# Performance work log

Measured on AMD Instinct MI355X. Metric: run time of the kernel, lower is better.

Reference implementation:

```python
import jax, jax.numpy as jnp
import numpy as np

N_USERS, N_ITEMS, DIM = 50000, 25000, 128
E_H, E_R = 600000, 1000000
N_LAYERS = 2


def setup_inputs() -> dict:
    key = jax.random.key(0)
    ks = jax.random.split(key, 20)
    nrm = lambda k, s: jax.random.normal(k, s, jnp.float32) * 0.05
    inp = {
        "u_emb": nrm(ks[0], (N_USERS, DIM)),
        "i_emb": nrm(ks[1], (N_ITEMS, DIM)),
        "gating_W": nrm(ks[2], (4, DIM, DIM)),
        "gating_b": jnp.zeros((4, DIM), jnp.float32),
        "attention": nrm(ks[3], (DIM,)),
        "attention_mat": nrm(ks[4], (DIM, DIM)),
    }
    for i, name in enumerate(["Hs", "Hj", "Hp"]):
        inp[name + "_row"] = jax.random.randint(ks[5 + 2 * i], (E_H,), 0, N_USERS, jnp.int32)
        inp[name + "_col"] = jax.random.randint(ks[6 + 2 * i], (E_H,), 0, N_USERS, jnp.int32)
        inp[name + "_val"] = jax.random.uniform(ks[11 + i], (E_H,), jnp.float32)
    inp["R_row"] = jax.random.randint(ks[14], (E_R,), 0, N_USERS, jnp.int32)
    inp["R_col"] = jax.random.randint(ks[15], (E_R,), 0, N_ITEMS, jnp.int32)
    inp["R_val"] = jnp.ones((E_R,), jnp.float32)
    return inp


def spmm(row, col, val, X, n_out):
    # sparse (n_out x n_in) @ dense (n_in x d), COO edge list form
    return jax.ops.segment_sum(val[:, None] * X[col], row, num_segments=n_out)


def l2norm(x):
    return x * jax.lax.rsqrt(jnp.maximum(jnp.sum(x * x, axis=1, keepdims=True), 1e-12))


def reference(u_emb, i_emb, gating_W, gating_b, attention, attention_mat,
              Hs_row, Hs_col, Hs_val, Hj_row, Hj_col, Hj_val,
              Hp_row, Hp_col, Hp_val, R_row, R_col, R_val):
    gate = lambda e, c: e * jax.nn.sigmoid(e @ gating_W[c] + gating_b[c])

    def chan_att(cs):
        # per-channel attention score: sum_d a_d * (E_c @ W_att)_d  -> [N, C]
        w = jnp.stack([jnp.sum(attention * (c @ attention_mat), axis=1) for c in cs], axis=1)
        s = jax.nn.softmax(w, axis=1)
        mixed = sum(s[:, k:k + 1] * cs[k] for k in range(len(cs)))
        return mixed, s

    H = [(Hs_row, Hs_col, Hs_val), (Hj_row, Hj_col, Hj_val), (Hp_row, Hp_col, Hp_val)]
    cur = [gate(u_emb, c) for c in range(3)]        # channel user embeddings
    cur_s = gate(u_emb, 3)                          # simple-gated user embeddings
    cur_i = i_emb
    all_c = [[cur[k]] for k in range(3)]
    all_i = [cur_i]
    all_s = [cur_s]
    for _ in range(N_LAYERS):
        mixed = chan_att(cur)[0] + cur_s / 2
        for k in range(3):
            r, c, v = H[k]
            cur[k] = spmm(r, c, v, cur[k], N_USERS)
            all_c[k].append(l2norm(cur[k]))
        new_item = spmm(R_col, R_row, R_val, mixed, N_ITEMS)   # R^T @ mixed
        all_i.append(l2norm(new_item))
        cur_s = spmm(R_row, R_col, R_val, cur_i, N_USERS)      # R @ item
        all_s.append(l2norm(cur_s))
        cur_i = new_item
    fc = [sum(all_c[k]) for k in range(3)]
    final_user = chan_att(fc)[0] + sum(all_s) / 2
    final_item = sum(all_i)
    return jnp.concatenate([final_user, final_item], axis=0)  # [N_USERS+N_ITEMS, DIM]
```

## Files before the change

kernel.cpp:

```cpp
#include <hip/hip_runtime.h>
#include <cstddef>
#include <cstdint>

#define NU 50000
#define NI 25000
#define DIMN 128
#define EH 600000
#define ER 1000000

typedef unsigned int u32;
typedef unsigned long long u64;
typedef unsigned char u8;
typedef __attribute__((ext_vector_type(8))) short short8;
typedef __attribute__((ext_vector_type(16))) float float16;

__device__ __forceinline__ float wave_sum64(float v) {
#pragma unroll
  for (int m = 32; m >= 1; m >>= 1) v += __shfl_xor(v, m, 64);
  return v;
}

__device__ __forceinline__ u32 pack_bf16x2(float a, float b) {
  u32 ua = __float_as_uint(a), ub = __float_as_uint(b);
  ua = (ua + 0x7fffu + ((ua >> 16) & 1u)) >> 16;
  ub = (ub + 0x7fffu + ((ub >> 16) & 1u)) >> 16;
  return ua | (ub << 16);
}
__device__ __forceinline__ u32 bf16_hi(float v) {
  u32 u = __float_as_uint(v);
  u = (u + 0x7fffu + ((u >> 16) & 1u)) & 0xffff0000u;
  return u;
}
__device__ __forceinline__ float blo(u32 p) { return __uint_as_float(p << 16); }
__device__ __forceinline__ float bhi(u32 p) { return __uint_as_float(p & 0xffff0000u); }

struct Graphs {
  const int* row[5];
  const int* col[5];
  const float* val[5];
};

__device__ __forceinline__ int g_E(int z) {
  const int E[5] = {EH, EH, EH, ER, ER};
  return E[z];
}

#define NBKU 196
#define TOTB (5 * NBKU)
#define CAPH 3584
#define CAPR 5632
#define CAPT 5632
#define ECAP 4315136
#define FCAP 5760
#define CHUNK 2048

__device__ __forceinline__ int capstart(int z, int b) {
  const int base[5] = {0, 702464, 1404928, 2107392, 3211264};
  const int cap[5] = {CAPH, CAPH, CAPH, CAPR, CAPT};
  return base[z] + b * cap[z];
}

__global__ __launch_bounds__(256) void k_prep(const float* __restrict__ U, u32* __restrict__ UP16,
                                              const float* __restrict__ IE,
                                              float* __restrict__ out_i, u32* __restrict__ IE16,
                                              const float* __restrict__ W, u32* __restrict__ W16,
                                              const float* __restrict__ attm,
                                              const float* __restrict__ att,
                                              float* __restrict__ attv) {
  int b = blockIdx.x;
  if (b < 12500) {
    int i = b * 256 + threadIdx.x;
    float2 v = ((const float2*)U)[i];
    UP16[i] = pack_bf16x2(v.x, v.y);
  } else if (b < 18750) {
    int i = (b - 12500) * 256 + threadIdx.x;
    float2 v = ((const float2*)IE)[i];
    ((float2*)out_i)[i] = v;
    IE16[i] = pack_bf16x2(v.x, v.y);
  } else if (b < 18878) {
    int i = (b - 18750) * 256 + threadIdx.x;
    int col = i & 127, k2 = (i >> 7) & 63, c = i >> 13;
    const float* Wc = W + (size_t)c * DIMN * DIMN;
    W16[i] = pack_bf16x2(Wc[(size_t)(2 * k2) * DIMN + col], Wc[(size_t)(2 * k2 + 1) * DIMN + col]);
  } else {
    int e = threadIdx.x;
    if (e < 128) {
      float s = 0.f;
      for (int d = 0; d < DIMN; ++d) s += attm[e * DIMN + d] * att[d];
      attv[e] = s;
    }
  }
}

__global__ __launch_bounds__(256) void k_gate(const u32* __restrict__ UP16,
                                              const u32* __restrict__ W16,
                                              const float* __restrict__ B, u32* S16, u32* G016,
                                              u32* G116, u32* G216) {
  int c = blockIdx.y;
  const u32* __restrict__ Wc = W16 + (size_t)c * (64 * 128);
  int r0 = blockIdx.x * 64;
  int t = threadIdx.x;
  int w = t >> 6, lane = t & 63;
  int ln = lane & 31, h = lane >> 5;
  int rh = w & 1, mh = w >> 1;

  __shared__ u32 ldsP[64 * 65];

  int rowl = rh * 32 + ln;
  int rg = r0 + rowl;
  int rc = (rg < NU) ? rg : (NU - 1);

  float16 acc[2];
#pragma unroll
  for (int m = 0; m < 2; ++m)
#pragma unroll
    for (int q = 0; q < 16; ++q) acc[m][q] = 0.f;

  const u32* __restrict__ urow = UP16 + (size_t)rc * 64;
#pragma unroll
  for (int kk = 0; kk < 8; ++kk) {
    int kw = kk * 8 + 4 * h;
    union {
      u32 u[4];
      short8 s;
    } bf;
#pragma unroll
    for (int j = 0; j < 4; ++j) bf.u[j] = urow[kw + j];
#pragma unroll
    for (int m = 0; m < 2; ++m) {
      union {
        u32 u[4];
        short8 s;
      } af;
      int col = 64 * mh + 32 * m + ln;
#pragma unroll
      for (int j = 0; j < 4; ++j) af.u[j] = Wc[(size_t)(kw + j) * DIMN + col];
      acc[m] = __builtin_amdgcn_mfma_f32_32x32x16_bf16(af.s, bf.s, acc[m], 0, 0, 0);
    }
  }
#pragma unroll
  for (int m = 0; m < 2; ++m)
#pragma unroll
    for (int q = 0; q < 16; q += 2) {
      int cw = 32 * mh + 16 * m + ((q & 3) >> 1) + 4 * (q >> 2) + 2 * h;
      ldsP[rowl * 65 + cw] = pack_bf16x2(acc[m][q], acc[m][q + 1]);
    }
  __syncthreads();

  int colw = t & 63, rloc = t >> 6;
  float bx = B[c * DIMN + 2 * colw], by = B[c * DIMN + 2 * colw + 1];
  u32* dst = (c == 0) ? G016 : (c == 1) ? G116 : (c == 2) ? G216 : S16;
#pragma unroll
  for (int i = 0; i < 16; ++i) {
    int row = i * 4 + rloc;
    int rg2 = r0 + row;
    if (rg2 >= NU) continue;
    u32 p = ldsP[row * 65 + colw];
    u32 uu = UP16[(size_t)rg2 * 64 + colw];
    float sx = 1.f / (1.f + __expf(-(blo(p) + bx)));
    float sy = 1.f / (1.f + __expf(-(bhi(p) + by)));
    dst[(size_t)rg2 * 64 + colw] = pack_bf16x2(blo(uu) * sx, bhi(uu) * sy);
  }
}

__global__ __launch_bounds__(256) void k_bscat(Graphs g, int* __restrict__ bcnt,
                                               u32* __restrict__ epb, u8* __restrict__ erb) {
  int z = blockIdx.y;
  int E = g_E(z);
  if ((int)(blockIdx.x * CHUNK) >= E) return;
  int sh = (z == 4) ? 7 : 8;
  int mask = (1 << sh) - 1;
  __shared__ int hist[2][NBKU], basel[NBKU], curl[2][NBKU], h0s[NBKU];
  for (int i = threadIdx.x; i < NBKU; i += 256) {
    hist[0][i] = 0;
    hist[1][i] = 0;
    curl[0][i] = 0;
    curl[1][i] = 0;
  }
  __syncthreads();
  const int* __restrict__ row = g.row[z];
  const int* __restrict__ col = g.col[z];
  const float* __restrict__ val = g.val[z];
  int e0 = blockIdx.x * CHUNK + threadIdx.x;
  int half = threadIdx.x >> 7;
  int r[8];
  u32 pay[8];
  bool ok[8];
#pragma unroll
  for (int k = 0; k < 8; ++k) {
    int e = e0 + k * 256;
    ok[k] = e < E;
    r[k] = ok[k] ? row[e] : 0;
    pay[k] = ok[k] ? (u32)col[e] : 0u;
  }
  if (z < 3) {
#pragma unroll
    for (int k = 0; k < 8; ++k) {
      int e = e0 + k * 256;
      if (ok[k]) pay[k] |= bf16_hi(val[e]);
    }
  }
#pragma unroll
  for (int k = 0; k < 8; ++k)
    if (ok[k]) atomicAdd(&hist[half][r[k] >> sh], 1);
  __syncthreads();
  for (int i = threadIdx.x; i < NBKU; i += 256) {
    int h0 = hist[0][i];
    int tot = h0 + hist[1][i];
    h0s[i] = h0;
    if (tot) basel[i] = capstart(z, i) + atomicAdd(&bcnt[z * NBKU + i], tot);
  }
  __syncthreads();
#pragma unroll
  for (int k = 0; k < 8; ++k)
    if (ok[k]) {
      int b = r[k] >> sh;
      int rank = atomicAdd(&curl[half][b], 1);
      int pos = basel[b] + (half ? h0s[b] : 0) + rank;
      epb[pos] = pay[k];
      erb[pos] = (u8)(r[k] & mask);
    }
}

__global__ __launch_bounds__(256) void k_fine(u32* __restrict__ epb, const u8* __restrict__ erb,
                                              const int* __restrict__ bcnt,
                                              int* __restrict__ ptr2) {
  int z = blockIdx.y, b = blockIdx.x, t = threadIdx.x;
  int sh = (z == 4) ? 7 : 8;
  int mask = (1 << sh) - 1;
  const int poffs2[5] = {0, 100000, 200000, 300000, 400000};
  const int nz[5] = {NU, NU, NU, NU, NI};
  int s = capstart(z, b);
  int n = bcnt[z * NBKU + b];
  __shared__ int cnt[256], scn[256], curl[256];
  __shared__ u32 buf[FCAP];
  cnt[t] = 0;
  curl[t] = 0;
  __syncthreads();
  for (int i = t; i < n; i += 256) atomicAdd(&cnt[erb[s + i]], 1);
  __syncthreads();
  int v = cnt[t];
  scn[t] = v;
  __syncthreads();
  for (int o = 1; o < 256; o <<= 1) {
    int x = (t >= o) ? scn[t - o] : 0;
    __syncthreads();
    scn[t] += x;
    __syncthreads();
  }
  int excl = scn[t] - v;
  __syncthreads();
  scn[t] = excl;
  int rg = (b << sh) + t;
  if (t <= mask && rg < nz[z]) {
    ptr2[poffs2[z] + 2 * rg] = s + excl;
    ptr2[poffs2[z] + 2 * rg + 1] = s + excl + v;
  }
  __syncthreads();
  for (int i = t; i < n; i += 256) {
    int r = erb[s + i];
    int rank = atomicAdd(&curl[r], 1);
    buf[scn[r] + rank] = epb[s + i];
  }
  __syncthreads();
  for (int i = t; i < n; i += 256) epb[s + i] = buf[i];
}

struct Job {
  const int* ptr2;
  const u32* X16;
  u32* Y16;
  float* ACCF;
  u32* ACC16;
  const u32* AINIT16;
  int nrows;
};

template <bool UNIT>
__device__ __forceinline__ void spmm_run(const u32* __restrict__ ep, const Job& jb) {
  int w = blockIdx.x * 4 + __builtin_amdgcn_readfirstlane(threadIdx.x >> 6);
  int lane = threadIdx.x & 63;
  if (w >= jb.nrows) return;
  const int2 pp = ((const int2*)jb.ptr2)[w];
  int s = __builtin_amdgcn_readfirstlane(pp.x);
  int t = __builtin_amdgcn_readfirstlane(pp.y);
  const char* __restrict__ Xb = (const char*)jb.X16;
  u32 lo4 = (u32)(lane << 2);
  float ax = 0.f, ay = 0.f;
  int e = s;
  for (; e + 8 <= t; e += 8) {
    u32 off[8];
    float vv[8];
#pragma unroll
    for (int k = 0; k < 8; ++k) {
      u32 q = ep[e + k];
      if (UNIT) {
        off[k] = (q << 8) | lo4;
      } else {
        off[k] = ((q & 0xffffu) << 8) | lo4;
        vv[k] = bhi(q);
      }
    }
    u32 p[8];
#pragma unroll
    for (int k = 0; k < 8; ++k) p[k] = *(const u32*)(Xb + off[k]);
#pragma unroll
    for (int k = 0; k < 8; ++k) {
      if (UNIT) {
        ax += blo(p[k]);
        ay += bhi(p[k]);
      } else {
        ax += vv[k] * blo(p[k]);
        ay += vv[k] * bhi(p[k]);
      }
    }
  }
  for (; e + 4 <= t; e += 4) {
    u32 off[4];
    float vv[4];
#pragma unroll
    for (int k = 0; k < 4; ++k) {
      u32 q = ep[e + k];
      if (UNIT) {
        off[k] = (q << 8) | lo4;
      } else {
        off[k] = ((q & 0xffffu) << 8) | lo4;
        vv[k] = bhi(q);
      }
    }
    u32 p[4];
#pragma unroll
    for (int k = 0; k < 4; ++k) p[k] = *(const u32*)(Xb + off[k]);
#pragma unroll
    for (int k = 0; k < 4; ++k) {
      if (UNIT) {
        ax += blo(p[k]);
        ay += bhi(p[k]);
      } else {
        ax += vv[k] * blo(p[k]);
        ay += vv[k] * bhi(p[k]);
      }
    }
  }
  for (; e < t; ++e) {
    u32 q = ep[e];
    u32 off;
    float v = 1.f;
    if (UNIT) {
      off = (q << 8) | lo4;
    } else {
      off = ((q & 0xffffu) << 8) | lo4;
      v = bhi(q);
    }
    u32 p = *(const u32*)(Xb + off);
    ax += v * blo(p);
    ay += v * bhi(p);
  }
  size_t b64 = (size_t)w * 64 + lane;
  if (jb.ACCF) {
    float ss = wave_sum64(ax * ax + ay * ay);
    float rs = rsqrtf(fmaxf(ss, 1e-12f));
    if (jb.Y16) jb.Y16[b64] = pack_bf16x2(ax, ay);
    float2 o = *(const float2*)(jb.ACCF + 2 * b64);
    o.x += ax * rs;
    o.y += ay * rs;
    *(float2*)(jb.ACCF + 2 * b64) = o;
  } else if (jb.ACC16) {
    float ss = wave_sum64(ax * ax + ay * ay);
    float rs = rsqrtf(fmaxf(ss, 1e-12f));
    u32 p = jb.AINIT16 ? jb.AINIT16[b64] : jb.ACC16[b64];
    float ox = blo(p) + ax * rs, oy = bhi(p) + ay * rs;
    if (jb.Y16) jb.Y16[b64] = pack_bf16x2(ax, ay);
    jb.ACC16[b64] = pack_bf16x2(ox, oy);
  } else if (jb.Y16) {
    jb.Y16[b64] = pack_bf16x2(ax, ay);
  }
}

__global__ __launch_bounds__(256) void k_spmm5(const u32* __restrict__ ep, Job j0, Job j1,
                                               Job j2, Job j3, Job j4) {
  int y = blockIdx.y;
  if (y < 2) {
    Job jb = (y == 0) ? j0 : j1;
    spmm_run<true>(ep, jb);
  } else {
    Job jb = (y == 2) ? j2 : (y == 3) ? j3 : j4;
    spmm_run<false>(ep, jb);
  }
}

template <bool OUT16>
__global__ __launch_bounds__(256) void k_mix(const u32* __restrict__ c0_,
                                             const u32* __restrict__ c1_,
                                             const u32* __restrict__ c2_,
                                             const u32* __restrict__ sp_,
                                             const float* __restrict__ attv, float* outf,
                                             u32* out16, int nrows) {
  int w = blockIdx.x * 4 + __builtin_amdgcn_readfirstlane(threadIdx.x >> 6);
  int lane = threadIdx.x & 63;
  if (w >= nrows) return;
  size_t b64 = (size_t)w * 64 + lane;
  u32 p0 = c0_[b64], p1 = c1_[b64], p2 = c2_[b64];
  float2 x0 = make_float2(blo(p0), bhi(p0));
  float2 x1 = make_float2(blo(p1), bhi(p1));
  float2 x2 = make_float2(blo(p2), bhi(p2));
  float2 av = *(const float2*)(attv + lane * 2);
  float w0 = wave_sum64(x0.x * av.x + x0.y * av.y);
  float w1 = wave_sum64(x1.x * av.x + x1.y * av.y);
  float w2 = wave_sum64(x2.x * av.x + x2.y * av.y);
  float m = fmaxf(w0, fmaxf(w1, w2));
  float e0 = __expf(w0 - m), e1 = __expf(w1 - m), e2 = __expf(w2 - m);
  float inv = 1.f / (e0 + e1 + e2);
  float s0 = e0 * inv, s1 = e1 * inv, s2 = e2 * inv;
  u32 ps = sp_[b64];
  float ox = s0 * x0.x + s1 * x1.x + s2 * x2.x + 0.5f * blo(ps);
  float oy = s0 * x0.y + s1 * x1.y + s2 * x2.y + 0.5f * bhi(ps);
  if (OUT16)
    out16[b64] = pack_bf16x2(ox, oy);
  else
    *(float2*)(outf + 2 * b64) = make_float2(ox, oy);
}

extern "C" void kernel_launch(void* const* d_in, const int* in_sizes, int n_in, void* d_out,
                              int out_size, void* d_ws, size_t ws_size, hipStream_t stream) {
  const float* u_emb = (const float*)d_in[0];
  const float* i_emb = (const float*)d_in[1];
  const float* gW = (const float*)d_in[2];
  const float* gB = (const float*)d_in[3];
  const float* att = (const float*)d_in[4];
  const float* attm = (const float*)d_in[5];
  Graphs g;
  g.row[0] = (const int*)d_in[6];
  g.col[0] = (const int*)d_in[7];
  g.val[0] = (const float*)d_in[8];
  g.row[1] = (const int*)d_in[9];
  g.col[1] = (const int*)d_in[10];
  g.val[1] = (const float*)d_in[11];
  g.row[2] = (const int*)d_in[12];
  g.col[2] = (const int*)d_in[13];
  g.val[2] = (const float*)d_in[14];
  g.row[3] = (const int*)d_in[15];
  g.col[3] = (const int*)d_in[16];
  g.val[3] = (const float*)d_in[17];
  g.row[4] = (const int*)d_in[16];
  g.col[4] = (const int*)d_in[15];
  g.val[4] = (const float*)d_in[17];

  const size_t U = (size_t)NU * DIMN, U64 = (size_t)NU * 64, I64 = (size_t)NI * 64;
  u32* G016 = (u32*)d_ws;
  u32* G116 = G016 + U64;
  u32* G216 = G116 + U64;
  u32* C1016 = G216 + U64;
  u32* C1116 = C1016 + U64;
  u32* C1216 = C1116 + U64;
  u32* GS016 = C1216 + U64;
  u32* GS116 = GS016 + U64;
  u32* GS216 = GS116 + U64;
  u32* MIX16 = GS216 + U64;
  u32* S16 = MIX16 + U64;
  u32* SACC = S16 + U64;
  u32* I116 = SACC + U64;
  u32* IE16 = I116 + I64;
  u32* UP16 = IE16 + I64;
  u32* W16 = UP16 + U64;
  float* attv = (float*)(W16 + 32768);
  int* ptr2 = (int*)(attv + DIMN);
  int* bcnt = ptr2 + 450000;
  uintptr_t a0 = ((uintptr_t)(bcnt + 984) + 15u) & ~(uintptr_t)15;
  u32* epb = (u32*)a0;
  u8* erb = (u8*)(epb + ECAP);
  float* out_u = (float*)d_out;
  float* out_i = out_u + U;

  const int CHB = (ER + CHUNK - 1) / CHUNK;
  const int GRID_U = (NU + 3) / 4;
  const int po1 = 100000, po2 = 200000, po3 = 300000, po4 = 400000;

  hipMemsetAsync(bcnt, 0, TOTB * sizeof(int), stream);
  hipLaunchKernelGGL(k_bscat, dim3(CHB, 5), dim3(256), 0, stream, g, bcnt, epb, erb);
  hipLaunchKernelGGL(k_fine, dim3(NBKU, 5), dim3(256), 0, stream, epb, erb, bcnt, ptr2);

  hipLaunchKernelGGL(k_prep, dim3(18879), dim3(256), 0, stream, u_emb, UP16, i_emb, out_i, IE16,
                     gW, W16, attm, att, attv);
  hipLaunchKernelGGL(k_gate, dim3((NU + 63) / 64, 4), dim3(256), 0, stream, UP16, W16, gB, S16,
                     G016, G116, G216);

  hipLaunchKernelGGL((k_mix<true>), dim3(GRID_U), dim3(256), 0, stream, G016, G116, G216, S16,
                     attv, (float*)nullptr, MIX16, NU);
  {
    Job j0 = {ptr2 + po3, IE16, S16, nullptr, SACC, S16, NU};
    Job j1 = {ptr2 + po4, MIX16, I116, out_i, nullptr, nullptr, NI};
    Job j2 = {ptr2, G016, C1016, nullptr, GS016, G016, NU};
    Job j3 = {ptr2 + po1, G116, C1116, nullptr, GS116, G116, NU};
    Job j4 = {ptr2 + po2, G216, C1216, nullptr, GS216, G216, NU};
    hipLaunchKernelGGL(k_spmm5, dim3(GRID_U, 5), dim3(256), 0, stream, epb, j0, j1, j2, j3, j4);
  }

  hipLaunchKernelGGL((k_mix<true>), dim3(GRID_U), dim3(256), 0, stream, C1016, C1116, C1216, S16,
                     attv, (float*)nullptr, MIX16, NU);
  {
    Job j0 = {ptr2 + po3, I116, nullptr, nullptr, SACC, nullptr, NU};
    Job j1 = {ptr2 + po4, MIX16, nullptr, out_i, nullptr, nullptr, NI};
    Job j2 = {ptr2, C1016, nullptr, nullptr, GS016, nullptr, NU};
    Job j3 = {ptr2 + po1, C1116, nullptr, nullptr, GS116, nullptr, NU};
    Job j4 = {ptr2 + po2, C1216, nullptr, nullptr, GS216, nullptr, NU};
    hipLaunchKernelGGL(k_spmm5, dim3(GRID_U, 5), dim3(256), 0, stream, epb, j0, j1, j2, j3, j4);
  }

  hipLaunchKernelGGL((k_mix<false>), dim3(GRID_U), dim3(256), 0, stream, GS016, GS116, GS216,
                     SACC, attv, out_u, (u32*)nullptr, NU);
}
```

Measured before the change: 533.9 us.

## Fuse graph bucketing with prep and fine sort with gating into two launches

```diff
diff --git a/kernel.cpp b/kernel.cpp
--- a/kernel.cpp
+++ b/kernel.cpp
@@ -54,31 +54,122 @@
 #define FCAP 5760
 #define CHUNK 2048
 
+#define BSH 293
+#define BSR 489
+#define B1SCAT (3 * BSH + 2 * BSR)
+#define B1PREP 18879
+#define B2FINE TOTB
+#define B2GATE (782 * 4)
+
 __device__ __forceinline__ int capstart(int z, int b) {
   const int base[5] = {0, 702464, 1404928, 2107392, 3211264};
   const int cap[5] = {CAPH, CAPH, CAPH, CAPR, CAPT};
   return base[z] + b * cap[z];
 }
 
-__global__ __launch_bounds__(256) void k_prep(const float* __restrict__ U, u32* __restrict__ UP16,
-                                              const float* __restrict__ IE,
-                                              float* __restrict__ out_i, u32* __restrict__ IE16,
-                                              const float* __restrict__ W, u32* __restrict__ W16,
-                                              const float* __restrict__ attm,
-                                              const float* __restrict__ att,
-                                              float* __restrict__ attv) {
+__global__ __launch_bounds__(256) void k_build1(Graphs g, int* __restrict__ bcnt,
+                                                u32* __restrict__ epb, u8* __restrict__ erb,
+                                                const float* __restrict__ U,
+                                                u32* __restrict__ UP16,
+                                                const float* __restrict__ IE,
+                                                u32* __restrict__ IE16,
+                                                const float* __restrict__ W,
+                                                u32* __restrict__ W16,
+                                                const float* __restrict__ attm,
+                                                const float* __restrict__ att,
+                                                float* __restrict__ attv) {
   int b = blockIdx.x;
-  if (b < 12500) {
-    int i = b * 256 + threadIdx.x;
+  if (b < B1SCAT) {
+    int z, cb;
+    if (b < 3 * BSH) {
+      z = b / BSH;
+      cb = b - z * BSH;
+    } else {
+      int r = b - 3 * BSH;
+      z = 3 + r / BSR;
+      cb = r - (z - 3) * BSR;
+    }
+    int E = g_E(z);
+    int sh = (z == 4) ? 7 : 8;
+    int mask = (1 << sh) - 1;
+    __shared__ int hist[2][NBKU], basel[NBKU], curl[2][NBKU], h0s[NBKU];
+    for (int i = threadIdx.x; i < NBKU; i += 256) {
+      hist[0][i] = 0;
+      hist[1][i] = 0;
+      curl[0][i] = 0;
+      curl[1][i] = 0;
+    }
+    __syncthreads();
+    const int* __restrict__ row = g.row[z];
+    const int* __restrict__ col = g.col[z];
+    const float* __restrict__ val = g.val[z];
+    int e0 = cb * CHUNK + threadIdx.x * 8;
+    int half = threadIdx.x >> 7;
+    int r[8];
+    u32 pay[8];
+    bool ok[8];
+    if (e0 + 8 <= E) {
+      int4 ra = *(const int4*)(row + e0);
+      int4 rb = *(const int4*)(row + e0 + 4);
+      int4 ca = *(const int4*)(col + e0);
+      int4 cbv = *(const int4*)(col + e0 + 4);
+      r[0] = ra.x; r[1] = ra.y; r[2] = ra.z; r[3] = ra.w;
+      r[4] = rb.x; r[5] = rb.y; r[6] = rb.z; r[7] = rb.w;
+      pay[0] = (u32)ca.x; pay[1] = (u32)ca.y; pay[2] = (u32)ca.z; pay[3] = (u32)ca.w;
+      pay[4] = (u32)cbv.x; pay[5] = (u32)cbv.y; pay[6] = (u32)cbv.z; pay[7] = (u32)cbv.w;
+#pragma unroll
+      for (int k = 0; k < 8; ++k) ok[k] = true;
+      if (z < 3) {
+        float4 va = *(const float4*)(val + e0);
+        float4 vb = *(const float4*)(val + e0 + 4);
+        pay[0] |= bf16_hi(va.x); pay[1] |= bf16_hi(va.y);
+        pay[2] |= bf16_hi(va.z); pay[3] |= bf16_hi(va.w);
+        pay[4] |= bf16_hi(vb.x); pay[5] |= bf16_hi(vb.y);
+        pay[6] |= bf16_hi(vb.z); pay[7] |= bf16_hi(vb.w);
+      }
+    } else {
+#pragma unroll
+      for (int k = 0; k < 8; ++k) {
+        int e = e0 + k;
+        ok[k] = e < E;
+        r[k] = ok[k] ? row[e] : 0;
+        pay[k] = ok[k] ? (u32)col[e] : 0u;
+        if (z < 3 && ok[k]) pay[k] |= bf16_hi(val[e]);
+      }
+    }
+#pragma unroll
+    for (int k = 0; k < 8; ++k)
+      if (ok[k]) atomicAdd(&hist[half][r[k] >> sh], 1);
+    __syncthreads();
+    for (int i = threadIdx.x; i < NBKU; i += 256) {
+      int h0 = hist[0][i];
+      int tot = h0 + hist[1][i];
+      h0s[i] = h0;
+      if (tot) basel[i] = capstart(z, i) + atomicAdd(&bcnt[z * NBKU + i], tot);
+    }
+    __syncthreads();
+#pragma unroll
+    for (int k = 0; k < 8; ++k)
+      if (ok[k]) {
+        int bb = r[k] >> sh;
+        int rank = atomicAdd(&curl[half][bb], 1);
+        int pos = basel[bb] + (half ? h0s[bb] : 0) + rank;
+        epb[pos] = pay[k];
+        erb[pos] = (u8)(r[k] & mask);
+      }
+    return;
+  }
+  int b2 = b - B1SCAT;
+  if (b2 < 12500) {
+    int i = b2 * 256 + threadIdx.x;
     float2 v = ((const float2*)U)[i];
     UP16[i] = pack_bf16x2(v.x, v.y);
-  } else if (b < 18750) {
-    int i = (b - 12500) * 256 + threadIdx.x;
+  } else if (b2 < 18750) {
+    int i = (b2 - 12500) * 256 + threadIdx.x;
     float2 v = ((const float2*)IE)[i];
-    ((float2*)out_i)[i] = v;
     IE16[i] = pack_bf16x2(v.x, v.y);
-  } else if (b < 18878) {
-    int i = (b - 18750) * 256 + threadIdx.x;
+  } else if (b2 < 18878) {
+    int i = (b2 - 18750) * 256 + threadIdx.x;
     int col = i & 127, k2 = (i >> 7) & 63, c = i >> 13;
     const float* Wc = W + (size_t)c * DIMN * DIMN;
     W16[i] = pack_bf16x2(Wc[(size_t)(2 * k2) * DIMN + col], Wc[(size_t)(2 * k2 + 1) * DIMN + col]);
@@ -92,19 +183,103 @@
   }
 }
 
-__global__ __launch_bounds__(256) void k_gate(const u32* __restrict__ UP16,
-                                              const u32* __restrict__ W16,
-                                              const float* __restrict__ B, u32* S16, u32* G016,
-                                              u32* G116, u32* G216) {
-  int c = blockIdx.y;
+struct FineLds {
+  int cnt[256];
+  int scn[256];
+  int curl[256];
+  u32 buf[FCAP];
+};
+struct GateLds {
+  u32 ldsP[64 * 65];
+};
+
+__global__ __launch_bounds__(256) void k_build2(u32* __restrict__ epb, const u8* __restrict__ erb,
+                                                const int* __restrict__ bcnt,
+                                                int* __restrict__ ptr2,
+                                                const u32* __restrict__ UP16,
+                                                const u32* __restrict__ W16,
+                                                const float* __restrict__ B, u32* S16,
+                                                u32* G016, u32* G116, u32* G216) {
+  __shared__ __align__(16) union {
+    FineLds f;
+    GateLds g;
+  } sh;
+  int b = blockIdx.x;
+  int t = threadIdx.x;
+  if (b < B2FINE) {
+    int z = b / NBKU, bb = b - z * NBKU;
+    int shf = (z == 4) ? 7 : 8;
+    int mask = (1 << shf) - 1;
+    const int poffs2[5] = {0, 100000, 200000, 300000, 400000};
+    const int nz[5] = {NU, NU, NU, NU, NI};
+    int s = capstart(z, bb);
+    int n = bcnt[z * NBKU + bb];
+    FineLds& L = sh.f;
+    L.cnt[t] = 0;
+    L.curl[t] = 0;
+    __syncthreads();
+    int n4 = n >> 2;
+    for (int i = t; i < n4; i += 256) {
+      u32 r4 = *(const u32*)(erb + s + 4 * i);
+      atomicAdd(&L.cnt[r4 & 255u], 1);
+      atomicAdd(&L.cnt[(r4 >> 8) & 255u], 1);
+      atomicAdd(&L.cnt[(r4 >> 16) & 255u], 1);
+      atomicAdd(&L.cnt[r4 >> 24], 1);
+    }
+    for (int i = 4 * n4 + t; i < n; i += 256) atomicAdd(&L.cnt[erb[s + i]], 1);
+    __syncthreads();
+    int v = L.cnt[t];
+    L.scn[t] = v;
+    __syncthreads();
+    for (int o = 1; o < 256; o <<= 1) {
+      int x = (t >= o) ? L.scn[t - o] : 0;
+      __syncthreads();
+      L.scn[t] += x;
+      __syncthreads();
+    }
+    int excl = L.scn[t] - v;
+    __syncthreads();
+    L.scn[t] = excl;
+    int rg = (bb << shf) + t;
+    if (t <= mask && rg < nz[z]) {
+      ptr2[poffs2[z] + 2 * rg] = s + excl;
+      ptr2[poffs2[z] + 2 * rg + 1] = s + excl + v;
+    }
+    __syncthreads();
+    for (int i = t; i < n4; i += 256) {
+      u32 r4 = *(const u32*)(erb + s + 4 * i);
+      uint4 p4 = *(const uint4*)(epb + s + 4 * i);
+      int r0 = (int)(r4 & 255u);
+      int k0 = atomicAdd(&L.curl[r0], 1);
+      L.buf[L.scn[r0] + k0] = p4.x;
+      int r1 = (int)((r4 >> 8) & 255u);
+      int k1 = atomicAdd(&L.curl[r1], 1);
+      L.buf[L.scn[r1] + k1] = p4.y;
+      int r2 = (int)((r4 >> 16) & 255u);
+      int k2 = atomicAdd(&L.curl[r2], 1);
+      L.buf[L.scn[r2] + k2] = p4.z;
+      int r3 = (int)(r4 >> 24);
+      int k3 = atomicAdd(&L.curl[r3], 1);
+      L.buf[L.scn[r3] + k3] = p4.w;
+    }
+    for (int i = 4 * n4 + t; i < n; i += 256) {
+      int r = erb[s + i];
+      int rank = atomicAdd(&L.curl[r], 1);
+      L.buf[L.scn[r] + rank] = epb[s + i];
+    }
+    __syncthreads();
+    for (int i = t; i < n4; i += 256) ((uint4*)(epb + s))[i] = ((const uint4*)L.buf)[i];
+    for (int i = 4 * n4 + t; i < n; i += 256) epb[s + i] = L.buf[i];
+    return;
+  }
+  int gb = b - B2FINE;
+  int c = gb / 782;
+  int r0 = (gb - c * 782) * 64;
   const u32* __restrict__ Wc = W16 + (size_t)c * (64 * 128);
-  int r0 = blockIdx.x * 64;
-  int t = threadIdx.x;
   int w = t >> 6, lane = t & 63;
   int ln = lane & 31, h = lane >> 5;
   int rh = w & 1, mh = w >> 1;
-
-  __shared__ u32 ldsP[64 * 65];
+  u32* ldsP = sh.g.ldsP;
 
   int rowl = rh * 32 + ln;
   int rg = r0 + rowl;
@@ -163,109 +338,6 @@
   }
 }
 
-__global__ __launch_bounds__(256) void k_bscat(Graphs g, int* __restrict__ bcnt,
-                                               u32* __restrict__ epb, u8* __restrict__ erb) {
-  int z = blockIdx.y;
-  int E = g_E(z);
-  if ((int)(blockIdx.x * CHUNK) >= E) return;
-  int sh = (z == 4) ? 7 : 8;
-  int mask = (1 << sh) - 1;
-  __shared__ int hist[2][NBKU], basel[NBKU], curl[2][NBKU], h0s[NBKU];
-  for (int i = threadIdx.x; i < NBKU; i += 256) {
-    hist[0][i] = 0;
-    hist[1][i] = 0;
-    curl[0][i] = 0;
-    curl[1][i] = 0;
-  }
-  __syncthreads();
-  const int* __restrict__ row = g.row[z];
-  const int* __restrict__ col = g.col[z];
-  const float* __restrict__ val = g.val[z];
-  int e0 = blockIdx.x * CHUNK + threadIdx.x;
-  int half = threadIdx.x >> 7;
-  int r[8];
-  u32 pay[8];
-  bool ok[8];
-#pragma unroll
-  for (int k = 0; k < 8; ++k) {
-    int e = e0 + k * 256;
-    ok[k] = e < E;
-    r[k] = ok[k] ? row[e] : 0;
-    pay[k] = ok[k] ? (u32)col[e] : 0u;
-  }
-  if (z < 3) {
-#pragma unroll
-    for (int k = 0; k < 8; ++k) {
-      int e = e0 + k * 256;
-      if (ok[k]) pay[k] |= bf16_hi(val[e]);
-    }
-  }
-#pragma unroll
-  for (int k = 0; k < 8; ++k)
-    if (ok[k]) atomicAdd(&hist[half][r[k] >> sh], 1);
-  __syncthreads();
-  for (int i = threadIdx.x; i < NBKU; i += 256) {
-    int h0 = hist[0][i];
-    int tot = h0 + hist[1][i];
-    h0s[i] = h0;
-    if (tot) basel[i] = capstart(z, i) + atomicAdd(&bcnt[z * NBKU + i], tot);
-  }
-  __syncthreads();
-#pragma unroll
-  for (int k = 0; k < 8; ++k)
-    if (ok[k]) {
-      int b = r[k] >> sh;
-      int rank = atomicAdd(&curl[half][b], 1);
-      int pos = basel[b] + (half ? h0s[b] : 0) + rank;
-      epb[pos] = pay[k];
-      erb[pos] = (u8)(r[k] & mask);
-    }
-}
-
-__global__ __launch_bounds__(256) void k_fine(u32* __restrict__ epb, const u8* __restrict__ erb,
-                                              const int* __restrict__ bcnt,
-                                              int* __restrict__ ptr2) {
-  int z = blockIdx.y, b = blockIdx.x, t = threadIdx.x;
-  int sh = (z == 4) ? 7 : 8;
-  int mask = (1 << sh) - 1;
-  const int poffs2[5] = {0, 100000, 200000, 300000, 400000};
-  const int nz[5] = {NU, NU, NU, NU, NI};
-  int s = capstart(z, b);
-  int n = bcnt[z * NBKU + b];
-  __shared__ int cnt[256], scn[256], curl[256];
-  __shared__ u32 buf[FCAP];
-  cnt[t] = 0;
-  curl[t] = 0;
-  __syncthreads();
-  for (int i = t; i < n; i += 256) atomicAdd(&cnt[erb[s + i]], 1);
-  __syncthreads();
-  int v = cnt[t];
-  scn[t] = v;
-  __syncthreads();
-  for (int o = 1; o < 256; o <<= 1) {
-    int x = (t >= o) ? scn[t - o] : 0;
-    __syncthreads();
-    scn[t] += x;
-    __syncthreads();
-  }
-  int excl = scn[t] - v;
-  __syncthreads();
-  scn[t] = excl;
-  int rg = (b << sh) + t;
-  if (t <= mask && rg < nz[z]) {
-    ptr2[poffs2[z] + 2 * rg] = s + excl;
-    ptr2[poffs2[z] + 2 * rg + 1] = s + excl + v;
-  }
-  __syncthreads();
-  for (int i = t; i < n; i += 256) {
-    int r = erb[s + i];
-    int rank = atomicAdd(&curl[r], 1);
-    buf[scn[r] + rank] = epb[s + i];
-  }
-  __syncthreads();
-  for (int i = t; i < n; i += 256) epb[s + i] = buf[i];
-}
-
 struct Job {
   const int* ptr2;
   const u32* X16;
@@ -273,6 +345,7 @@
   float* ACCF;
   u32* ACC16;
   const u32* AINIT16;
+  const float* AINITF;
   int nrows;
 };
 
@@ -361,7 +434,11 @@
     float ss = wave_sum64(ax * ax + ay * ay);
     float rs = rsqrtf(fmaxf(ss, 1e-12f));
     if (jb.Y16) jb.Y16[b64] = pack_bf16x2(ax, ay);
-    float2 o = *(const float2*)(jb.ACCF + 2 * b64);
+    float2 o;
+    if (jb.AINITF)
+      o = *(const float2*)(jb.AINITF + 2 * b64);
+    else
+      o = *(const float2*)(jb.ACCF + 2 * b64);
     o.x += ax * rs;
     o.y += ay * rs;
     *(float2*)(jb.ACCF + 2 * b64) = o;
@@ -472,38 +549,34 @@
   float* out_u = (float*)d_out;
   float* out_i = out_u + U;
 
-  const int CHB = (ER + CHUNK - 1) / CHUNK;
   const int GRID_U = (NU + 3) / 4;
   const int po1 = 100000, po2 = 200000, po3 = 300000, po4 = 400000;
 
   hipMemsetAsync(bcnt, 0, TOTB * sizeof(int), stream);
-  hipLaunchKernelGGL(k_bscat, dim3(CHB, 5), dim3(256), 0, stream, g, bcnt, epb, erb);
-  hipLaunchKernelGGL(k_fine, dim3(NBKU, 5), dim3(256), 0, stream, epb, erb, bcnt, ptr2);
-
-  hipLaunchKernelGGL(k_prep, dim3(18879), dim3(256), 0, stream, u_emb, UP16, i_emb, out_i, IE16,
-                     gW, W16, attm, att, attv);
-  hipLaunchKernelGGL(k_gate, dim3((NU + 63) / 64, 4), dim3(256), 0, stream, UP16, W16, gB, S16,
-                     G016, G116, G216);
+  hipLaunchKernelGGL(k_build1, dim3(B1SCAT + B1PREP), dim3(256), 0, stream, g, bcnt, epb, erb,
+                     u_emb, UP16, i_emb, IE16, gW, W16, attm, att, attv);
+  hipLaunchKernelGGL(k_build2, dim3(B2FINE + B2GATE), dim3(256), 0, stream, epb, erb, bcnt, ptr2,
+                     UP16, W16, gB, S16, G016, G116, G216);
 
   hipLaunchKernelGGL((k_mix<true>), dim3(GRID_U), dim3(256), 0, stream, G016, G116, G216, S16,
                      attv, (float*)nullptr, MIX16, NU);
   {
-    Job j0 = {ptr2 + po3, IE16, S16, nullptr, SACC, S16, NU};
-    Job j1 = {ptr2 + po4, MIX16, I116, out_i, nullptr, nullptr, NI};
-    Job j2 = {ptr2, G016, C1016, nullptr, GS016, G016, NU};
-    Job j3 = {ptr2 + po1, G116, C1116, nullptr, GS116, G116, NU};
-    Job j4 = {ptr2 + po2, G216, C1216, nullptr, GS216, G216, NU};
+    Job j0 = {ptr2 + po3, IE16, S16, nullptr, SACC, S16, nullptr, NU};
+    Job j1 = {ptr2 + po4, MIX16, I116, out_i, nullptr, nullptr, i_emb, NI};
+    Job j2 = {ptr2, G016, C1016, nullptr, GS016, G016, nullptr, NU};
+    Job j3 = {ptr2 + po1, G116, C1116, nullptr, GS116, G116, nullptr, NU};
+    Job j4 = {ptr2 + po2, G216, C1216, nullptr, GS216, G216, nullptr, NU};
     hipLaunchKernelGGL(k_spmm5, dim3(GRID_U, 5), dim3(256), 0, stream, epb, j0, j1, j2, j3, j4);
   }
 
   hipLaunchKernelGGL((k_mix<true>), dim3(GRID_U), dim3(256), 0, stream, C1016, C1116, C1216, S16,
                      attv, (float*)nullptr, MIX16, NU);
   {
-    Job j0 = {ptr2 + po3, I116, nullptr, nullptr, SACC, nullptr, NU};
-    Job j1 = {ptr2 + po4, MIX16, nullptr, out_i, nullptr, nullptr, NI};
-    Job j2 = {ptr2, C1016, nullptr, nullptr, GS016, nullptr, NU};
-    Job j3 = {ptr2 + po1, C1116, nullptr, nullptr, GS116, nullptr, NU};
-    Job j4 = {ptr2 + po2, C1216, nullptr, nullptr, GS216, nullptr, NU};
+    Job j0 = {ptr2 + po3, I116, nullptr, nullptr, SACC, nullptr, nullptr, NU};
+    Job j1 = {ptr2 + po4, MIX16, nullptr, out_i, nullptr, nullptr, nullptr, NI};
+    Job j2 = {ptr2, C1016, nullptr, nullptr, GS016, nullptr, nullptr, NU};
+    Job j3 = {ptr2 + po1, C1116, nullptr, nullptr, GS116, nullptr, nullptr, NU};
+    Job j4 = {ptr2 + po2, C1216, nullptr, nullptr, GS216, nullptr, nullptr, NU};
     hipLaunchKernelGGL(k_spmm5, dim3(GRID_U, 5), dim3(256), 0, stream, epb, j0, j1, j2, j3, j4);
   }
 
```

New measurement: 495.2 us. 7.2% less time.
